# Kernel tuning notes

Measured on AMD Instinct MI355X. Metric: run time of the kernel, lower is better.

The kernel has to match this reference:

```python
import jax, jax.numpy as jnp
import numpy as np
from jax import lax

B, T = 2048, 256
V, E, H = 128, 128, 64
POS_WEIGHT = 20.0


def setup_inputs() -> dict:
    key = jax.random.key(0)
    ks = jax.random.split(key, 9)
    # indices in [1, V) so padding_idx=0 row (zeroed) is unused
    x = jax.random.randint(ks[0], (B, T), 1, V)
    targets = (jax.random.uniform(ks[1], (B,)) < 0.05).astype(jnp.float32)
    emb = jax.random.normal(ks[2], (V, E), dtype=jnp.float32).at[0].set(0.0)  # padding_idx=0
    k = 1.0 / np.sqrt(H)
    W_ih = jax.random.uniform(ks[3], (4 * H, E), minval=-k, maxval=k, dtype=jnp.float32)
    W_hh = jax.random.uniform(ks[4], (4 * H, H), minval=-k, maxval=k, dtype=jnp.float32)
    b_ih = jax.random.uniform(ks[5], (4 * H,), minval=-k, maxval=k, dtype=jnp.float32)
    b_hh = jax.random.uniform(ks[6], (4 * H,), minval=-k, maxval=k, dtype=jnp.float32)
    W_fc = jax.random.uniform(ks[7], (1, H), minval=-k, maxval=k, dtype=jnp.float32)
    b_fc = jax.random.uniform(ks[8], (1,), minval=-k, maxval=k, dtype=jnp.float32)
    return {"x": x, "targets": targets, "emb": emb, "W_ih": W_ih, "W_hh": W_hh,
            "b_ih": b_ih, "b_hh": b_hh, "W_fc": W_fc, "b_fc": b_fc}


def reference(x, targets, emb, W_ih, W_hh, b_ih, b_hh, W_fc, b_fc):
    xe = emb[x]  # [B, T, E]
    # precompute input-to-hidden projections for all timesteps: [B, T, 4H]
    xp = jnp.einsum('bte,ge->btg', xe, W_ih) + b_ih + b_hh
    h0 = jnp.zeros((xe.shape[0], W_hh.shape[1]), dtype=xe.dtype)
    c0 = jnp.zeros_like(h0)

    def step(carry, xt):
        h, c = carry
        gates = xt + h @ W_hh.T  # [B, 4H], PyTorch gate order: i, f, g, o
        i, f, g, o = jnp.split(gates, 4, axis=-1)
        c = jax.nn.sigmoid(f) * c + jax.nn.sigmoid(i) * jnp.tanh(g)
        h = jax.nn.sigmoid(o) * jnp.tanh(c)
        return (h, c), None

    (hT, _), _ = lax.scan(step, (h0, c0), jnp.swapaxes(xp, 0, 1))  # scan over time
    logits = (hT @ W_fc.T + b_fc)[:, 0]  # [B]
    # BCEWithLogits with pos_weight, mean reduction (numerically stable)
    loss = -(POS_WEIGHT * targets * jax.nn.log_sigmoid(logits)
             + (1.0 - targets) * jax.nn.log_sigmoid(-logits)).mean()
    return logits, loss
```

## Files before the change

kernel.cpp:

```cpp
#include <hip/hip_runtime.h>
#include <stdint.h>

#define B_ 2048
#define T_ 256
#define V_ 128
#define E_ 128
#define H_ 64
#define G4_ 256
#define POS_W 20.0f
#define MB_ 8
#define NBLK_ (B_ / MB_)
typedef _Float16 half1;
typedef __attribute__((ext_vector_type(8))) _Float16 f16x8;
typedef __attribute__((ext_vector_type(4))) float f32x4;

#if __has_builtin(__builtin_amdgcn_exp2f)
#define EXP2F(x) __builtin_amdgcn_exp2f(x)
#else
#define EXP2F(x) exp2f(x)
#endif

#if __has_builtin(__builtin_amdgcn_rcpf)
#define RCPF(x) __builtin_amdgcn_rcpf(x)
#else
#define RCPF(x) (1.0f / (x))
#endif

__device__ __forceinline__ float sigm(float x) {
    return RCPF(1.0f + EXP2F(-1.44269504f * x));
}
__device__ __forceinline__ float tanhr(float x) {
    float t = EXP2F(2.88539008f * x);
    return 1.0f - 2.0f * RCPF(t + 1.0f);
}

__device__ __forceinline__ void lds_barrier() {
    asm volatile("s_waitcnt lgkmcnt(0)\n\ts_barrier" ::: "memory");
}

__global__ void k_prep(const float* __restrict__ emb, const float* __restrict__ Wih,
                       const float* __restrict__ bih, const float* __restrict__ bhh,
                       float* __restrict__ projC, float* __restrict__ loss_slot) {
    int tid = threadIdx.x;
    int v = blockIdx.x;
    if (v == 0 && tid == 0) *loss_slot = 0.0f;
    int u = tid >> 2, g = tid & 3;
    int row = g * 64 + u;
    const float4* e4 = (const float4*)(emb + v * E_);
    const float4* w4 = (const float4*)(Wih + row * E_);
    float acc = bih[row] + bhh[row];
#pragma unroll
    for (int i = 0; i < E_ / 4; ++i) {
        float4 a = e4[i];
        float4 b = w4[i];
        acc += a.x * b.x + a.y * b.y + a.z * b.z + a.w * b.w;
    }
    projC[v * G4_ + tid] = acc;
}

__launch_bounds__(256, 1)
__global__ void k_lstm(const int* __restrict__ x, const float* __restrict__ Whh,
                       const float* __restrict__ projC, const float* __restrict__ Wfc,
                       const float* __restrict__ bfc, const float* __restrict__ targets,
                       float* __restrict__ logits, float* __restrict__ loss_slot) {
    int b0 = blockIdx.x * MB_;
    int t = threadIdx.x;
    int w = t >> 6, l = t & 63;
    int q = l >> 4, cc = l & 15;
    int u = 16 * w + cc;

    __shared__ __align__(16) half1 hf[2][1024];
    __shared__ int xT[T_][MB_];
    __shared__ float hfin[MB_][68];
    __shared__ float zred[MB_];

#pragma unroll
    for (int i = 0; i < MB_; ++i) xT[t][i] = x[(b0 + i) * T_ + t];
    ((float*)hf)[t] = 0.0f;
    ((float*)hf)[t + 256] = 0.0f;
    ((float*)hf)[t + 512] = 0.0f;
    ((float*)hf)[t + 768] = 0.0f;
    __syncthreads();

    f16x8 bf[4][2];
#pragma unroll
    for (int jj = 0; jj < 4; ++jj) {
#pragma unroll
        for (int c = 0; c < 2; ++c) {
            int row = jj * 64 + 16 * w + cc;
            int kb = c * 32 + q * 8;
            float4 w0 = *(const float4*)(Whh + row * H_ + kb);
            float4 w1 = *(const float4*)(Whh + row * H_ + kb + 4);
            f16x8 tmp;
            tmp[0] = (half1)w0.x; tmp[1] = (half1)w0.y;
            tmp[2] = (half1)w0.z; tmp[3] = (half1)w0.w;
            tmp[4] = (half1)w1.x; tmp[5] = (half1)w1.y;
            tmp[6] = (half1)w1.z; tmp[7] = (half1)w1.w;
            bf[jj][c] = tmp;
        }
    }

    int hbase = (u >> 5) * 512 + ((u >> 3) & 3) * 128 + (4 * q) * 8 + (u & 7);

    float cA = 0.0f, hA = 0.0f;
    float cB = 0.0f, hB = 0.0f;

    f32x4 ppA = *(const f32x4*)(projC + xT[0][q] * G4_ + u * 4);
    f32x4 ppB = *(const f32x4*)(projC + xT[0][q + 4] * G4_ + u * 4);
    f32x4 pnA = *(const f32x4*)(projC + xT[1][q] * G4_ + u * 4);
    f32x4 pnB = *(const f32x4*)(projC + xT[1][q + 4] * G4_ + u * 4);

    int p = 0;
#pragma unroll 2
    for (int step = 0; step < T_; ++step) {
        int t2 = (step + 2) & (T_ - 1);
        f32x4 p2A = *(const f32x4*)(projC + xT[t2][q] * G4_ + u * 4);
        f32x4 p2B = *(const f32x4*)(projC + xT[t2][q + 4] * G4_ + u * 4);

        const f16x8 a0 = *(const f16x8*)(hf[p] + l * 8);
        const f16x8 a1 = *(const f16x8*)(hf[p] + 512 + l * 8);

        f32x4 z4 = {0.0f, 0.0f, 0.0f, 0.0f};
        float gA[4], gB[4];
#pragma unroll
        for (int jj = 0; jj < 4; ++jj) {
            f32x4 d0 = __builtin_amdgcn_mfma_f32_16x16x32_f16(a0, bf[jj][0], z4, 0, 0, 0);
            f32x4 d = __builtin_amdgcn_mfma_f32_16x16x32_f16(a1, bf[jj][1], d0, 0, 0, 0);
            gA[jj] = d[0];
            gB[jj] = d[1];
        }

        float iA = sigm(gA[0] + ppA.x);
        float fA = sigm(gA[1] + ppA.y);
        float ggA = tanhr(gA[2] + ppA.z);
        float oA = sigm(gA[3] + ppA.w);
        cA = fA * cA + iA * ggA;
        hA = oA * tanhr(cA);

        float iB = sigm(gB[0] + ppB.x);
        float fB = sigm(gB[1] + ppB.y);
        float ggB = tanhr(gB[2] + ppB.z);
        float oB = sigm(gB[3] + ppB.w);
        cB = fB * cB + iB * ggB;
        hB = oB * tanhr(cB);

        hf[p ^ 1][hbase] = (half1)hA;
        hf[p ^ 1][hbase + 8] = (half1)hB;

        ppA = pnA; ppB = pnB;
        pnA = p2A; pnB = p2B;
        p ^= 1;
        lds_barrier();
    }

    hfin[q][u] = hA;
    hfin[q + 4][u] = hB;
    __syncthreads();
    int m4 = t >> 6, uu = t & 63;
    float wv = Wfc[uu];
    float pa = hfin[m4][uu] * wv;
    float pb = hfin[m4 + 4][uu] * wv;
#pragma unroll
    for (int off = 32; off > 0; off >>= 1) {
        pa += __shfl_down(pa, off, 64);
        pb += __shfl_down(pb, off, 64);
    }
    if (uu == 0) {
        float z = pa + bfc[0];
        logits[b0 + m4] = z;
        float tg = targets[b0 + m4];
        float e = EXP2F(-1.44269504f * fabsf(z));
        float lsp = fminf(z, 0.0f) - log1pf(e);
        float lsn = lsp - z;
        zred[m4] = -(POS_W * tg * lsp + (1.0f - tg) * lsn) * (1.0f / (float)B_);

        float z2 = pb + bfc[0];
        logits[b0 + m4 + 4] = z2;
        float tg2 = targets[b0 + m4 + 4];
        float e2 = EXP2F(-1.44269504f * fabsf(z2));
        float lsp2 = fminf(z2, 0.0f) - log1pf(e2);
        float lsn2 = lsp2 - z2;
        zred[m4 + 4] = -(POS_W * tg2 * lsp2 + (1.0f - tg2) * lsn2) * (1.0f / (float)B_);
    }
    __syncthreads();
    if (t == 0) {
        float s = 0.0f;
#pragma unroll
        for (int i = 0; i < MB_; ++i) s += zred[i];
        atomicAdd(loss_slot, s);
    }
}

extern "C" void kernel_launch(void* const* d_in, const int* in_sizes, int n_in,
                              void* d_out, int out_size, void* d_ws, size_t ws_size,
                              hipStream_t stream) {
    const int* x = (const int*)d_in[0];
    const float* targets = (const float*)d_in[1];
    const float* emb = (const float*)d_in[2];
    const float* Wih = (const float*)d_in[3];
    const float* Whh = (const float*)d_in[4];
    const float* bih = (const float*)d_in[5];
    const float* bhh = (const float*)d_in[6];
    const float* Wfc = (const float*)d_in[7];
    const float* bfc = (const float*)d_in[8];
    float* out = (float*)d_out;

    float* projC = (float*)d_ws;

    k_prep<<<dim3(V_), dim3(256), 0, stream>>>(emb, Wih, bih, bhh, projC, out + B_);
    k_lstm<<<dim3(NBLK_), dim3(256), 0, stream>>>(x, Whh, projC, Wfc, bfc, targets, out,
                                                  out + B_);
}
```

Before: 170.3 us.

## Shorten LSTM step critical path with independent MFMAs and prescaled gate inputs

```diff
diff --git a/kernel.cpp b/kernel.cpp
--- a/kernel.cpp
+++ b/kernel.cpp
@@ -26,13 +26,7 @@
 #define RCPF(x) (1.0f / (x))
 #endif
 
-__device__ __forceinline__ float sigm(float x) {
-    return RCPF(1.0f + EXP2F(-1.44269504f * x));
-}
-__device__ __forceinline__ float tanhr(float x) {
-    float t = EXP2F(2.88539008f * x);
-    return 1.0f - 2.0f * RCPF(t + 1.0f);
-}
+#define L2E 1.44269504f
 
 __device__ __forceinline__ void lds_barrier() {
     asm volatile("s_waitcnt lgkmcnt(0)\n\ts_barrier" ::: "memory");
@@ -75,7 +69,7 @@
     __shared__ float zred[MB_];
 
 #pragma unroll
-    for (int i = 0; i < MB_; ++i) xT[t][i] = x[(b0 + i) * T_ + t];
+    for (int i = 0; i < MB_; ++i) xT[t][i] = x[(b0 + i) * T_ + t] << 10;
     ((float*)hf)[t] = 0.0f;
     ((float*)hf)[t + 256] = 0.0f;
     ((float*)hf)[t + 512] = 0.0f;
@@ -104,51 +98,72 @@
 
     float cA = 0.0f, hA = 0.0f;
     float cB = 0.0f, hB = 0.0f;
-
-    f32x4 ppA = *(const f32x4*)(projC + xT[0][q] * G4_ + u * 4);
-    f32x4 ppB = *(const f32x4*)(projC + xT[0][q + 4] * G4_ + u * 4);
-    f32x4 pnA = *(const f32x4*)(projC + xT[1][q] * G4_ + u * 4);
-    f32x4 pnB = *(const f32x4*)(projC + xT[1][q + 4] * G4_ + u * 4);
-
+    const char* pcb = (const char*)projC;
+    int uoff = u << 4;
+
+    f32x4 ppA = *(const f32x4*)(pcb + xT[0][q] + uoff);
+    f32x4 ppB = *(const f32x4*)(pcb + xT[0][q + 4] + uoff);
+    f32x4 pnA = *(const f32x4*)(pcb + xT[1][q] + uoff);
+    f32x4 pnB = *(const f32x4*)(pcb + xT[1][q + 4] + uoff);
+    int xcA = xT[2][q];
+    int xcB = xT[2][q + 4];
+
+    const f32x4 z4 = {0.0f, 0.0f, 0.0f, 0.0f};
     int p = 0;
 #pragma unroll 2
     for (int step = 0; step < T_; ++step) {
-        int t2 = (step + 2) & (T_ - 1);
-        f32x4 p2A = *(const f32x4*)(projC + xT[t2][q] * G4_ + u * 4);
-        f32x4 p2B = *(const f32x4*)(projC + xT[t2][q + 4] * G4_ + u * 4);
-
         const f16x8 a0 = *(const f16x8*)(hf[p] + l * 8);
         const f16x8 a1 = *(const f16x8*)(hf[p] + 512 + l * 8);
 
-        f32x4 z4 = {0.0f, 0.0f, 0.0f, 0.0f};
-        float gA[4], gB[4];
+        f32x4 d0[4], d1[4];
 #pragma unroll
         for (int jj = 0; jj < 4; ++jj) {
-            f32x4 d0 = __builtin_amdgcn_mfma_f32_16x16x32_f16(a0, bf[jj][0], z4, 0, 0, 0);
-            f32x4 d = __builtin_amdgcn_mfma_f32_16x16x32_f16(a1, bf[jj][1], d0, 0, 0, 0);
-            gA[jj] = d[0];
-            gB[jj] = d[1];
+            d0[jj] = __builtin_amdgcn_mfma_f32_16x16x32_f16(a0, bf[jj][0], z4, 0, 0, 0);
+            d1[jj] = __builtin_amdgcn_mfma_f32_16x16x32_f16(a1, bf[jj][1], z4, 0, 0, 0);
         }
 
-        float iA = sigm(gA[0] + ppA.x);
-        float fA = sigm(gA[1] + ppA.y);
-        float ggA = tanhr(gA[2] + ppA.z);
-        float oA = sigm(gA[3] + ppA.w);
-        cA = fA * cA + iA * ggA;
-        hA = oA * tanhr(cA);
-
-        float iB = sigm(gB[0] + ppB.x);
-        float fB = sigm(gB[1] + ppB.y);
-        float ggB = tanhr(gB[2] + ppB.z);
-        float oB = sigm(gB[3] + ppB.w);
-        cB = fB * cB + iB * ggB;
-        hB = oB * tanhr(cB);
+        f32x4 p2A = *(const f32x4*)(pcb + xcA + uoff);
+        f32x4 p2B = *(const f32x4*)(pcb + xcB + uoff);
+        int xnA = xT[(step + 3) & (T_ - 1)][q];
+        int xnB = xT[(step + 3) & (T_ - 1)][q + 4];
+        float psAx = -L2E * ppA.x, psBx = -L2E * ppB.x;
+        float psAy = -L2E * ppA.y, psBy = -L2E * ppB.y;
+        float pgAz = 2.0f * L2E * ppA.z, pgBz = 2.0f * L2E * ppB.z;
+        float psAw = -L2E * ppA.w, psBw = -L2E * ppB.w;
+
+        float gA0 = d0[0][0] + d1[0][0], gB0 = d0[0][1] + d1[0][1];
+        float gA1 = d0[1][0] + d1[1][0], gB1 = d0[1][1] + d1[1][1];
+        float gA2 = d0[2][0] + d1[2][0], gB2 = d0[2][1] + d1[2][1];
+        float gA3 = d0[3][0] + d1[3][0], gB3 = d0[3][1] + d1[3][1];
+
+        float eiA = EXP2F(__builtin_fmaf(-L2E, gA0, psAx));
+        float eiB = EXP2F(__builtin_fmaf(-L2E, gB0, psBx));
+        float efA = EXP2F(__builtin_fmaf(-L2E, gA1, psAy));
+        float efB = EXP2F(__builtin_fmaf(-L2E, gB1, psBy));
+        float egA = EXP2F(__builtin_fmaf(2.0f * L2E, gA2, pgAz));
+        float egB = EXP2F(__builtin_fmaf(2.0f * L2E, gB2, pgBz));
+        float eoA = EXP2F(__builtin_fmaf(-L2E, gA3, psAw));
+        float eoB = EXP2F(__builtin_fmaf(-L2E, gB3, psBw));
+
+        float iA = RCPF(1.0f + eiA), iB = RCPF(1.0f + eiB);
+        float fA = RCPF(1.0f + efA), fB = RCPF(1.0f + efB);
+        float tgA = 1.0f - 2.0f * RCPF(egA + 1.0f);
+        float tgB = 1.0f - 2.0f * RCPF(egB + 1.0f);
+        float oA = RCPF(1.0f + eoA), oB = RCPF(1.0f + eoB);
+
+        cA = __builtin_fmaf(fA, cA, iA * tgA);
+        cB = __builtin_fmaf(fB, cB, iB * tgB);
+        float etA = EXP2F(2.0f * L2E * cA);
+        float etB = EXP2F(2.0f * L2E * cB);
+        hA = oA * (1.0f - 2.0f * RCPF(etA + 1.0f));
+        hB = oB * (1.0f - 2.0f * RCPF(etB + 1.0f));
 
         hf[p ^ 1][hbase] = (half1)hA;
         hf[p ^ 1][hbase + 8] = (half1)hB;
 
         ppA = pnA; ppB = pnB;
         pnA = p2A; pnB = p2B;
+        xcA = xnA; xcB = xnB;
         p ^= 1;
         lds_barrier();
     }
@@ -169,7 +184,7 @@
         float z = pa + bfc[0];
         logits[b0 + m4] = z;
         float tg = targets[b0 + m4];
-        float e = EXP2F(-1.44269504f * fabsf(z));
+        float e = EXP2F(-L2E * fabsf(z));
         float lsp = fminf(z, 0.0f) - log1pf(e);
         float lsn = lsp - z;
         zred[m4] = -(POS_W * tg * lsp + (1.0f - tg) * lsn) * (1.0f / (float)B_);
@@ -177,7 +192,7 @@
         float z2 = pb + bfc[0];
         logits[b0 + m4 + 4] = z2;
         float tg2 = targets[b0 + m4 + 4];
-        float e2 = EXP2F(-1.44269504f * fabsf(z2));
+        float e2 = EXP2F(-L2E * fabsf(z2));
         float lsp2 = fminf(z2, 0.0f) - log1pf(e2);
         float lsn2 = lsp2 - z2;
         zred[m4 + 4] = -(POS_W * tg2 * lsp2 + (1.0f - tg2) * lsn2) * (1.0f / (float)B_);
```

After: 166.6 us. -2.2%, faster.
